# Optimization experiments

Measured on AMD Instinct MI355X. Metric: run time of the kernel, lower is better.

The kernel has to match this reference:

```python
import jax, jax.numpy as jnp
import numpy as np
from jax import lax

# Surrogate spike: forward = Heaviside, backward = g / (1 + 5|x|)^2
@jax.custom_vjp
def spike_fn(x):
    return (x >= 0).astype(x.dtype)

def _spk_fwd(x):
    return spike_fn(x), x

def _spk_bwd(x, g):
    return (g / (1.0 + 5.0 * jnp.abs(x)) ** 2,)

spike_fn.defvjp(_spk_fwd, _spk_bwd)

BN_EPS = 1e-5

def _batchnorm(x, scale, bias, mean, var):
    # x: (B, C, T); eval-mode BN with running stats
    inv = scale / jnp.sqrt(var + BN_EPS)
    return x * inv[None, :, None] + (bias - mean * inv)[None, :, None]

def _conv1d(x, w, b, pad):
    y = lax.conv_general_dilated(x, w, (1,), [(pad, pad)],
                                 dimension_numbers=('NCH', 'OIH', 'NCH'))
    return y + b[None, :, None]

def setup_inputs() -> dict:
    key = jax.random.key(0)
    ks = jax.random.split(key, 12)
    B, T, EEG, GEO, TH, H, OUT = 4096, 320, 64, 18, 32, 16, 4
    inp = {
        'x_eeg': jax.random.normal(ks[0], (B, T, EEG), jnp.float32),
        'x_geo': jax.random.normal(ks[1], (B, T, GEO), jnp.float32),
        'conv1_w': jax.random.normal(ks[2], (TH, EEG, 5), jnp.float32) * 0.05,
        'conv1_b': jnp.zeros((TH,), jnp.float32),
        'bn1_s': jnp.ones((TH,), jnp.float32),
        'bn1_b': jnp.zeros((TH,), jnp.float32),
        'bn1_m': jnp.zeros((TH,), jnp.float32),
        'bn1_v': jnp.ones((TH,), jnp.float32),
        'conv2_w': jax.random.normal(ks[3], (H, TH, 3), jnp.float32) * 0.1,
        'conv2_b': jnp.zeros((H,), jnp.float32),
        'bn2_s': jnp.ones((H,), jnp.float32),
        'bn2_b': jnp.zeros((H,), jnp.float32),
        'bn2_m': jnp.zeros((H,), jnp.float32),
        'bn2_v': jnp.ones((H,), jnp.float32),
        'geo_w': jax.random.normal(ks[4], (H, GEO), jnp.float32) * 0.2,
        'geo_b': jnp.zeros((H,), jnp.float32),
        'gamma': jnp.full((H,), 0.5, jnp.float32),
        'fc1_w': jax.random.normal(ks[5], (64, 160), jnp.float32) * 0.08,
        'fc1_b': jnp.zeros((64,), jnp.float32),
        'fc2_w': jax.random.normal(ks[6], (OUT, 64), jnp.float32) * 0.12,
        'fc2_b': jnp.zeros((OUT,), jnp.float32),
    }
    return inp

def reference(x_eeg, x_geo, conv1_w, conv1_b, bn1_s, bn1_b, bn1_m, bn1_v,
              conv2_w, conv2_b, bn2_s, bn2_b, bn2_m, bn2_v,
              geo_w, geo_b, gamma, fc1_w, fc1_b, fc2_w, fc2_b):
    B, T, _ = x_eeg.shape
    theta_0, beta, tau_a, tau_m = 0.5, 1.8, 0.36, 0.8

    # EEG temporal encoder (eval mode: dropout = identity)
    h = x_eeg.transpose(0, 2, 1)  # (B, 64, T)
    h = jax.nn.relu(_batchnorm(_conv1d(h, conv1_w, conv1_b, 2), bn1_s, bn1_b, bn1_m, bn1_v))
    h = jax.nn.relu(_batchnorm(_conv1d(h, conv2_w, conv2_b, 1), bn2_s, bn2_b, bn2_m, bn2_v))
    eeg_encoded = h.transpose(0, 2, 1)  # (B, T, 16)

    geo_mod = jax.nn.sigmoid(jnp.einsum('bti,hi->bth', x_geo, geo_w) + geo_b)  # (B, T, 16)

    H = eeg_encoded.shape[-1]
    zeros = jnp.zeros((B, H), x_eeg.dtype)
    init = (zeros, zeros, zeros, zeros)  # mem_alif, eta, mem_li, prev_spk

    def step(carry, xs):
        mem_alif, eta, mem_li, prev_spk = carry
        cur_eeg, cur_geo = xs
        eta = tau_a * eta + (1.0 - tau_a) * prev_spk
        theta_t = theta_0 + beta * eta - gamma * cur_geo
        mem_alif = tau_m * mem_alif + cur_eeg
        spk = spike_fn(mem_alif - theta_t)
        mem_alif = mem_alif * (1.0 - spk)
        mem_li = 0.9 * mem_li + spk
        return (mem_alif, eta, mem_li, spk), mem_li

    xs = (eeg_encoded.transpose(1, 0, 2), geo_mod.transpose(1, 0, 2))  # (T, B, 16)
    _, pot = lax.scan(step, init, xs)  # (T, B, 16)

    pot = pot.transpose(1, 2, 0)                 # (B, 16, T)
    windows = pot.reshape(B, H, 10, 32)          # T = 320 = 10*32
    dp_feat = (windows[..., 16:].mean(-1) - windows[..., :16].mean(-1)).reshape(B, -1)  # (B, 160)

    out = jax.nn.relu(dp_feat @ fc1_w.T + fc1_b) @ fc2_w.T + fc2_b  # (B, 4)
    return out
```

## Files before the change

### kernel.cpp

```cpp
#include <hip/hip_runtime.h>
#include <math.h>

#define TB    4096
#define TSEQ  320
#define NEEG  64
#define NTH   32
#define NH    16
#define NGEO  18
#define TILE_T 48
#define NTILES 7
#define XROWS2 54
#define H1ROWS 50

typedef _Float16 f16x8 __attribute__((ext_vector_type(8)));
typedef _Float16 f16x2 __attribute__((ext_vector_type(2)));
typedef float f32x4 __attribute__((ext_vector_type(4)));
#define INV2048 4.8828125e-4f

#define OFF_W1F  0
#define OFF_W2F  10240
#define OFF_B1   11776
#define OFF_B2   11808
#define OFF_GWT  11824
#define OFF_FC1T 12112
#define OFF_FC2T 22352
#define OFF_ZP   22656
#define OFF_E    32768
#define SZ_EC    (TB*TSEQ*NH)
#define OFF_C    (OFF_E + SZ_EC)
#define OFF_DP   (OFF_C + SZ_EC)
#define SZ_DP    (TB*160)
#define REQ_FLOATS ((size_t)OFF_DP + SZ_DP)
#define REQ_BYTES  (REQ_FLOATS * 4)

__global__ void __launch_bounds__(256)
prep_kernel(const float* __restrict__ c1w, const float* __restrict__ c1b,
            const float* __restrict__ s1,  const float* __restrict__ bb1,
            const float* __restrict__ mm1, const float* __restrict__ vv1,
            const float* __restrict__ c2w, const float* __restrict__ c2b,
            const float* __restrict__ s2,  const float* __restrict__ bb2,
            const float* __restrict__ mm2, const float* __restrict__ vv2,
            const float* __restrict__ gw,  const float* __restrict__ fc1w,
            const float* __restrict__ fc2w, float* __restrict__ ws)
{
    const int tid = threadIdx.x;
    _Float16* w1fp = reinterpret_cast<_Float16*>(ws + OFF_W1F);
    _Float16* w2fp = reinterpret_cast<_Float16*>(ws + OFF_W2F);

    for (int d = tid; d < 10240; d += 256) {
        int j = d & 7, l = (d >> 3) & 63, nbk = d >> 9;
        int kk = nbk >> 1, nb = nbk & 1;
        int k = kk >> 1, i = (kk & 1) * 32 + ((l >> 4) * 8) + j;
        int c = nb * 16 + (l & 15);
        float inv = s1[c] / sqrtf(vv1[c] + 1e-5f);
        float wv = c1w[c * 320 + i * 5 + k] * inv;
        _Float16 hi = (_Float16)wv;
        _Float16 lo = (_Float16)((wv - (float)hi) * 2048.f);
        w1fp[((nbk * 2 + 0) * 64 + l) * 8 + j] = hi;
        w1fp[((nbk * 2 + 1) * 64 + l) * 8 + j] = lo;
    }
    for (int d = tid; d < 1536; d += 256) {
        int j = d & 7, l = (d >> 3) & 63, kk2 = d >> 9;
        int c = (l >> 4) * 8 + j;
        int o = l & 15;
        float inv = s2[o] / sqrtf(vv2[o] + 1e-5f);
        float wv = c2w[o * 96 + c * 3 + kk2] * inv;
        _Float16 hi = (_Float16)wv;
        _Float16 lo = (_Float16)((wv - (float)hi) * 2048.f);
        w2fp[((kk2 * 2 + 0) * 64 + l) * 8 + j] = hi;
        w2fp[((kk2 * 2 + 1) * 64 + l) * 8 + j] = lo;
    }
    if (tid < NTH) {
        float inv = s1[tid] / sqrtf(vv1[tid] + 1e-5f);
        ws[OFF_B1 + tid] = c1b[tid] * inv + bb1[tid] - mm1[tid] * inv;
    }
    if (tid < NH) {
        float inv = s2[tid] / sqrtf(vv2[tid] + 1e-5f);
        ws[OFF_B2 + tid] = c2b[tid] * inv + bb2[tid] - mm2[tid] * inv;
    }
    for (int d = tid; d < NGEO * NH; d += 256) {
        int i = d / NH, h = d - i * NH;
        ws[OFF_GWT + d] = gw[h * NGEO + i];
    }
    for (int d = tid; d < 160 * 64; d += 256) {
        int f = d / 64, o = d - f * 64;
        ws[OFF_FC1T + d] = fc1w[o * 160 + f];
    }
    if (tid < 256) {
        int j = tid / 4, o = tid - j * 4;
        ws[OFF_FC2T + tid] = fc2w[o * 64 + j];
    }
    if (tid < 64) ws[OFF_ZP + tid] = 0.f;
}

__global__ void __launch_bounds__(256, 2)
convm_kernel(const float* __restrict__ xeeg, const float* __restrict__ xgeo,
             const float* __restrict__ ws,   const float* __restrict__ geo_b,
             const float* __restrict__ gamma,
             float* __restrict__ E, float* __restrict__ C)
{
    __shared__ __align__(16) float xbuf[2][XROWS2 * 64];
    __shared__ __align__(16) float xg32[14 * 64];
    __shared__ __align__(16) _Float16 w2f[3][2][64][8];
    __shared__ __align__(16) _Float16 h1h[H1ROWS * 32];
    __shared__ __align__(16) _Float16 h1l[H1ROWS * 32];
    __shared__ __align__(16) float gws[NGEO * NH];
    __shared__ float b1s[32], b2s[16], gbs[16], gams[16];

    const int b = blockIdx.x, tid = threadIdx.x;
    const int l = tid & 63, w = tid >> 6;
    const int lrow = l & 15, lkg = l >> 4;
    const int nb = w >> 1, wsub = w & 1;
    const int ug = tid >> 2, hq = tid & 3;

    const float* xb  = xeeg + (size_t)b * TSEQ * NEEG;
    const float* xgb = xgeo + (size_t)b * TSEQ * NGEO;
    const float* zp  = ws + OFF_ZP;

#define STAGE_DMA(buf, t0n) do {                                                     \
        for (int c_ = w; c_ < XROWS2; c_ += 4) {                                     \
            int tg_ = (t0n) - 3 + c_;                                                \
            const float* s_ = (tg_ >= 0 && tg_ < TSEQ)                               \
                              ? (xb + (size_t)tg_ * 64 + l) : zp;                    \
            __builtin_amdgcn_global_load_lds(                                        \
                (const __attribute__((address_space(1))) void*)s_,                   \
                (__attribute__((address_space(3))) void*)&xbuf[(buf)][c_ * 64],      \
                4, 0, 0);                                                            \
        }                                                                            \
        for (int c_ = w; c_ < 14; c_ += 4) {                                         \
            int fo_ = (t0n) * NGEO + c_ * 64;                                        \
            const float* s_ = (fo_ < TSEQ * NGEO) ? (xgb + fo_ + l) : zp;            \
            __builtin_amdgcn_global_load_lds(                                        \
                (const __attribute__((address_space(1))) void*)s_,                   \
                (__attribute__((address_space(3))) void*)&xg32[c_ * 64],             \
                4, 0, 0);                                                            \
        }                                                                            \
    } while (0)

    f16x8 B1h[10], B1l[10];
    {
        const f16x8* wsrc = reinterpret_cast<const f16x8*>(ws + OFF_W1F);
        #pragma unroll
        for (int kk = 0; kk < 10; ++kk) {
            B1h[kk] = wsrc[((kk * 2 + nb) * 2 + 0) * 64 + l];
            B1l[kk] = wsrc[((kk * 2 + nb) * 2 + 1) * 64 + l];
        }
    }
    {
        const float4* s2 = reinterpret_cast<const float4*>(ws + OFF_W2F);
        float4* d2 = reinterpret_cast<float4*>(&w2f[0][0][0][0]);
        for (int p = tid; p < 384; p += 256) d2[p] = s2[p];
        if (tid < 32) b1s[tid] = ws[OFF_B1 + tid];
        if (tid < 16) {
            b2s[tid] = ws[OFF_B2 + tid];
            gbs[tid] = geo_b[tid];
            gams[tid] = gamma[tid];
        }
        for (int p = tid; p < NGEO * NH; p += 256) gws[p] = ws[OFF_GWT + p];
    }
    STAGE_DMA(0, 0);
    __syncthreads();

    for (int jt = 0; jt < NTILES; ++jt) {
        const int t0 = jt * TILE_T;
        const int cur = jt & 1;
        _Float16* xh = reinterpret_cast<_Float16*>(&xbuf[cur][0]);
        _Float16* xl = xh + XROWS2 * 64;

        float2 xr2[7];
        #pragma unroll
        for (int q = 0; q < 7; ++q) {
            int p = tid + q * 256;
            if (p < XROWS2 * 32) {
                int xr = p >> 5, ip = (p & 31) * 2;
                xr2[q] = *reinterpret_cast<const float2*>(&xbuf[cur][xr * 64 + ip]);
            }
        }
        if (ug < TILE_T && t0 + ug < TSEQ) {
            float z0 = gbs[hq * 4 + 0], z1 = gbs[hq * 4 + 1];
            float z2 = gbs[hq * 4 + 2], z3 = gbs[hq * 4 + 3];
            const float* xgr = &xg32[ug * NGEO];
            #pragma unroll
            for (int ii = 0; ii < NGEO; ++ii) {
                float xv = xgr[ii];
                float4 wv = *reinterpret_cast<const float4*>(&gws[ii * 16 + hq * 4]);
                z0 = fmaf(xv, wv.x, z0);
                z1 = fmaf(xv, wv.y, z1);
                z2 = fmaf(xv, wv.z, z2);
                z3 = fmaf(xv, wv.w, z3);
            }
            const int t4o = (t0 + ug) >> 2, tt = ug & 3;
            float* cp = C + (((size_t)t4o * TB + b) * 16 + hq * 4) * 4 + tt;
            cp[0]  = gams[hq * 4 + 0] * (1.f / (1.f + expf(-z0)));
            cp[4]  = gams[hq * 4 + 1] * (1.f / (1.f + expf(-z1)));
            cp[8]  = gams[hq * 4 + 2] * (1.f / (1.f + expf(-z2)));
            cp[12] = gams[hq * 4 + 3] * (1.f / (1.f + expf(-z3)));
        }
        __syncthreads();

        #pragma unroll
        for (int q = 0; q < 7; ++q) {
            int p = tid + q * 256;
            if (p < XROWS2 * 32) {
                int xr = p >> 5, ip = (p & 31) * 2;
                float f0 = xr2[q].x, f1 = xr2[q].y;
                _Float16 h0 = (_Float16)f0, h1v = (_Float16)f1;
                f16x2 vh = {h0, h1v};
                f16x2 vl = {(_Float16)((f0 - (float)h0) * 2048.f),
                            (_Float16)((f1 - (float)h1v) * 2048.f)};
                int idx = xr * 64 + (((ip >> 3) ^ (xr & 7)) << 3) + (ip & 7);
                *reinterpret_cast<f16x2*>(&xh[idx]) = vh;
                *reinterpret_cast<f16x2*>(&xl[idx]) = vl;
            }
        }
        __syncthreads();

        if (jt + 1 < NTILES) STAGE_DMA(cur ^ 1, (jt + 1) * TILE_T);
        __builtin_amdgcn_s_setprio(1);
        {
            const float bia = b1s[nb * 16 + lrow];
            #pragma unroll
            for (int pi = 0; pi < 2; ++pi) {
                const int mb = wsub + pi * 2;
                const int mbase = mb * 16;
                int s = mbase + lrow; if (s > H1ROWS - 1) s = H1ROWS - 1;
                f32x4 aH = {0.f, 0.f, 0.f, 0.f};
                f32x4 aM = aH, aL = aH;
                #pragma unroll
                for (int kk = 0; kk < 10; ++kk) {
                    const int xr = s + (kk >> 1);
                    const int gx = (kk & 1) * 4 + lkg;
                    const int off = xr * 64 + ((gx ^ (xr & 7)) << 3);
                    f16x8 Ah = *reinterpret_cast<const f16x8*>(&xh[off]);
                    f16x8 Al = *reinterpret_cast<const f16x8*>(&xl[off]);
                    aH = __builtin_amdgcn_mfma_f32_16x16x32_f16(Ah, B1h[kk], aH, 0, 0, 0);
                    aM = __builtin_amdgcn_mfma_f32_16x16x32_f16(Ah, B1l[kk], aM, 0, 0, 0);
                    aL = __builtin_amdgcn_mfma_f32_16x16x32_f16(Al, B1h[kk], aL, 0, 0, 0);
                }
                #pragma unroll
                for (int r = 0; r < 4; ++r) {
                    int so = mbase + lkg * 4 + r;
                    if (so < H1ROWS) {
                        int tg = t0 - 1 + so;
                        bool v = (tg >= 0 && tg < TSEQ);
                        float val = v ? fmaxf(fmaf(aM[r] + aL[r], INV2048, aH[r]) + bia, 0.f) : 0.f;
                        int key = (so >> 1) & 3;
                        int g = (nb * 2 + (lrow >> 3)) ^ key;
                        int idx = so * 32 + (g << 3) + (lrow & 7);
                        _Float16 hh = (_Float16)val;
                        h1h[idx] = hh;
                        h1l[idx] = (_Float16)((val - (float)hh) * 2048.f);
                    }
                }
            }
        }
        __builtin_amdgcn_s_setprio(0);
        __syncthreads();

        if (w < 3 && t0 + w * 16 < TSEQ) {
            const int ub = w * 16;
            f32x4 aH = {0.f, 0.f, 0.f, 0.f};
            f32x4 aM = aH, aL = aH;
            __builtin_amdgcn_s_setprio(1);
            #pragma unroll
            for (int kk = 0; kk < 3; ++kk) {
                int srow = ub + lrow + kk;
                int off = srow * 32 + ((lkg ^ ((srow >> 1) & 3)) << 3);
                f16x8 Ah = *reinterpret_cast<const f16x8*>(&h1h[off]);
                f16x8 Al = *reinterpret_cast<const f16x8*>(&h1l[off]);
                f16x8 Bh = *reinterpret_cast<const f16x8*>(&w2f[kk][0][l][0]);
                f16x8 Bl = *reinterpret_cast<const f16x8*>(&w2f[kk][1][l][0]);
                aH = __builtin_amdgcn_mfma_f32_16x16x32_f16(Ah, Bh, aH, 0, 0, 0);
                aM = __builtin_amdgcn_mfma_f32_16x16x32_f16(Ah, Bl, aM, 0, 0, 0);
                aL = __builtin_amdgcn_mfma_f32_16x16x32_f16(Al, Bh, aL, 0, 0, 0);
            }
            __builtin_amdgcn_s_setprio(0);
            const float bia = b2s[lrow];
            float4 ev;
            float* evp = reinterpret_cast<float*>(&ev);
            #pragma unroll
            for (int r = 0; r < 4; ++r)
                evp[r] = fmaxf(fmaf(aM[r] + aL[r], INV2048, aH[r]) + bia, 0.f);
            const int t4o = ((t0 + ub) >> 2) + lkg;
            float* ep = E + (((size_t)t4o * TB + b) * 16 + lrow) * 4;
            *reinterpret_cast<float4*>(ep) = ev;
        }
    }
#undef STAGE_DMA
}

__global__ void __launch_bounds__(256)
scan_kernel(const float* __restrict__ E, const float* __restrict__ C,
            float* __restrict__ DP)
{
    const int tid = threadIdx.x;
    const int h = tid & 15;
    const int b = blockIdx.x * 16 + (tid >> 4);
    const float4* e4 = reinterpret_cast<const float4*>(E);
    const float4* c4 = reinterpret_cast<const float4*>(C);
    const size_t idx = (size_t)b * 16 + h;
    const size_t slab = (size_t)TB * 16;

    float eta = 0.f, memv = 0.f, li = 0.f, ps = 0.f, accF = 0.f, accS = 0.f;
    float4 ev = e4[idx], cv = c4[idx];
    for (int t4 = 0; t4 < 80; ++t4) {
        float4 en, cn;
        if (t4 < 79) { en = e4[(size_t)(t4 + 1) * slab + idx]; cn = c4[(size_t)(t4 + 1) * slab + idx]; }
        const float* evp = reinterpret_cast<const float*>(&ev);
        const float* cvp = reinterpret_cast<const float*>(&cv);
        #pragma unroll
        for (int tt = 0; tt < 4; ++tt) {
            float e = evp[tt], c = cvp[tt];
            eta = 0.36f * eta + 0.64f * ps;
            float theta = 0.5f + 1.8f * eta - c;
            memv = 0.8f * memv + e;
            float spk = (memv - theta >= 0.f) ? 1.f : 0.f;
            memv *= (1.f - spk);
            li = 0.9f * li + spk;
            ps = spk;
            int t = t4 * 4 + tt;
            if (((t >> 4) & 1) == 0) accF += li; else accS += li;
        }
        if ((t4 & 7) == 7) {
            DP[(size_t)b * 160 + h * 10 + (t4 >> 3)] = (accS - accF) * 0.0625f;
            accF = 0.f; accS = 0.f;
        }
        ev = en; cv = cn;
    }
}

__global__ void __launch_bounds__(256)
fc_kernel(const float* __restrict__ DP, const float* __restrict__ ws,
          const float* __restrict__ fc1_b, const float* __restrict__ fc2_b,
          float* __restrict__ out)
{
    __shared__ float sh_dp[4][160];
    __shared__ float mid[4][64];
    const int tid = threadIdx.x;
    const int b0 = blockIdx.x * 4;
    for (int p = tid; p < 640; p += 256)
        sh_dp[p / 160][p - (p / 160) * 160] = DP[(size_t)b0 * 160 + p];
    __syncthreads();
    {
        const int bl = tid >> 6, o = tid & 63;
        const float* __restrict__ fc1t = ws + OFF_FC1T;
        float z = fc1_b[o];
        for (int f = 0; f < 160; ++f) z = fmaf(sh_dp[bl][f], fc1t[f * 64 + o], z);
        mid[bl][o] = fmaxf(z, 0.f);
    }
    __syncthreads();
    if (tid < 16) {
        const int bl = tid >> 2, oo = tid & 3;
        const float* __restrict__ fc2t = ws + OFF_FC2T;
        float z = fc2_b[oo];
        #pragma unroll
        for (int jj = 0; jj < 64; ++jj) z = fmaf(mid[bl][jj], fc2t[jj * 4 + oo], z);
        out[(size_t)(b0 + bl) * 4 + oo] = z;
    }
}

extern "C" void kernel_launch(void* const* d_in, const int* in_sizes, int n_in,
                              void* d_out, int out_size, void* d_ws, size_t ws_size,
                              hipStream_t stream)
{
    const float* xeeg = (const float*)d_in[0];
    const float* xgeo = (const float*)d_in[1];
    const float* c1w  = (const float*)d_in[2];
    const float* c1b  = (const float*)d_in[3];
    const float* s1   = (const float*)d_in[4];
    const float* bb1  = (const float*)d_in[5];
    const float* mm1  = (const float*)d_in[6];
    const float* vv1  = (const float*)d_in[7];
    const float* c2w  = (const float*)d_in[8];
    const float* c2b  = (const float*)d_in[9];
    const float* s2   = (const float*)d_in[10];
    const float* bb2  = (const float*)d_in[11];
    const float* mm2  = (const float*)d_in[12];
    const float* vv2  = (const float*)d_in[13];
    const float* gw   = (const float*)d_in[14];
    const float* gb   = (const float*)d_in[15];
    const float* gam  = (const float*)d_in[16];
    const float* fc1w = (const float*)d_in[17];
    const float* fc1b = (const float*)d_in[18];
    const float* fc2w = (const float*)d_in[19];
    const float* fc2b = (const float*)d_in[20];
    float* ws   = (float*)d_ws;
    float* outp = (float*)d_out;

    hipLaunchKernelGGL(prep_kernel, dim3(1), dim3(256), 0, stream,
                       c1w, c1b, s1, bb1, mm1, vv1, c2w, c2b, s2, bb2, mm2, vv2,
                       gw, fc1w, fc2w, ws);

    float* E  = ws + OFF_E;
    float* C  = ws + OFF_C;
    float* DP = ws + OFF_DP;
    hipLaunchKernelGGL(convm_kernel, dim3(TB), dim3(256), 0, stream,
                       xeeg, xgeo, ws, gb, gam, E, C);
    hipLaunchKernelGGL(scan_kernel, dim3(TB / 16), dim3(256), 0, stream,
                       E, C, DP);
    hipLaunchKernelGGL(fc_kernel, dim3(TB / 4), dim3(256), 0, stream,
                       DP, ws, fc1b, fc2b, outp);
}
```

Measured before the change: 337.0 us.

## Fuse spiking scan into conv kernel via LDS and enlarge time tile

Removes the separate scan kernel and the E/C intermediate global buffers. The conv kernel now writes the encoded EEG and geo modulation per tile into LDS, and 16 threads run the recurrent ALIF scan in-block, writing DP directly. The time tile grows from 48 to 64 so five tiles cover the sequence exactly, with an extra conv1 M-block alternated between warps. This saves global write/read traffic of two large tensors, but serializes the scan on 16 lanes inside each block, which may stall the conv pipeline and raise LDS use that could hurt occupancy.

```diff
diff --git a/kernel.cpp b/kernel.cpp
--- a/kernel.cpp
+++ b/kernel.cpp
@@ -7,10 +7,10 @@
 #define NTH   32
 #define NH    16
 #define NGEO  18
-#define TILE_T 48
-#define NTILES 7
-#define XROWS2 54
-#define H1ROWS 50
+#define TILE_T 64
+#define NTILES 5
+#define XROWS2 70
+#define H1ROWS 66
 
 typedef _Float16 f16x8 __attribute__((ext_vector_type(8)));
 typedef _Float16 f16x2 __attribute__((ext_vector_type(2)));
@@ -25,13 +25,7 @@
 #define OFF_FC1T 12112
 #define OFF_FC2T 22352
 #define OFF_ZP   22656
-#define OFF_E    32768
-#define SZ_EC    (TB*TSEQ*NH)
-#define OFF_C    (OFF_E + SZ_EC)
-#define OFF_DP   (OFF_C + SZ_EC)
-#define SZ_DP    (TB*160)
-#define REQ_FLOATS ((size_t)OFF_DP + SZ_DP)
-#define REQ_BYTES  (REQ_FLOATS * 4)
+#define OFF_DPF  32768
 
 __global__ void __launch_bounds__(256)
 prep_kernel(const float* __restrict__ c1w, const float* __restrict__ c1b,
@@ -96,14 +90,15 @@
 __global__ void __launch_bounds__(256, 2)
 convm_kernel(const float* __restrict__ xeeg, const float* __restrict__ xgeo,
              const float* __restrict__ ws,   const float* __restrict__ geo_b,
-             const float* __restrict__ gamma,
-             float* __restrict__ E, float* __restrict__ C)
+             const float* __restrict__ gamma, float* __restrict__ DP)
 {
     __shared__ __align__(16) float xbuf[2][XROWS2 * 64];
-    __shared__ __align__(16) float xg32[14 * 64];
+    __shared__ __align__(16) float xg32[18 * 64];
     __shared__ __align__(16) _Float16 w2f[3][2][64][8];
     __shared__ __align__(16) _Float16 h1h[H1ROWS * 32];
     __shared__ __align__(16) _Float16 h1l[H1ROWS * 32];
+    __shared__ __align__(16) float E_lds[TILE_T][20];
+    __shared__ __align__(16) float C_lds[2][TILE_T][20];
     __shared__ __align__(16) float gws[NGEO * NH];
     __shared__ float b1s[32], b2s[16], gbs[16], gams[16];
 
@@ -127,9 +122,8 @@
                 (__attribute__((address_space(3))) void*)&xbuf[(buf)][c_ * 64],      \
                 4, 0, 0);                                                            \
         }                                                                            \
-        for (int c_ = w; c_ < 14; c_ += 4) {                                         \
-            int fo_ = (t0n) * NGEO + c_ * 64;                                        \
-            const float* s_ = (fo_ < TSEQ * NGEO) ? (xgb + fo_ + l) : zp;            \
+        for (int c_ = w; c_ < 18; c_ += 4) {                                         \
+            const float* s_ = xgb + (size_t)(t0n) * NGEO + c_ * 64 + l;              \
             __builtin_amdgcn_global_load_lds(                                        \
                 (const __attribute__((address_space(1))) void*)s_,                   \
                 (__attribute__((address_space(3))) void*)&xg32[c_ * 64],             \
@@ -158,6 +152,8 @@
         }
         for (int p = tid; p < NGEO * NH; p += 256) gws[p] = ws[OFF_GWT + p];
     }
+    float eta = 0.f, memv = 0.f, li = 0.f, ps = 0.f, accF = 0.f, accS = 0.f;
+
     STAGE_DMA(0, 0);
     __syncthreads();
 
@@ -167,16 +163,16 @@
         _Float16* xh = reinterpret_cast<_Float16*>(&xbuf[cur][0]);
         _Float16* xl = xh + XROWS2 * 64;
 
-        float2 xr2[7];
+        float2 xr2[9];
         #pragma unroll
-        for (int q = 0; q < 7; ++q) {
+        for (int q = 0; q < 9; ++q) {
             int p = tid + q * 256;
             if (p < XROWS2 * 32) {
                 int xr = p >> 5, ip = (p & 31) * 2;
                 xr2[q] = *reinterpret_cast<const float2*>(&xbuf[cur][xr * 64 + ip]);
             }
         }
-        if (ug < TILE_T && t0 + ug < TSEQ) {
+        {
             float z0 = gbs[hq * 4 + 0], z1 = gbs[hq * 4 + 1];
             float z2 = gbs[hq * 4 + 2], z3 = gbs[hq * 4 + 3];
             const float* xgr = &xg32[ug * NGEO];
@@ -189,17 +185,17 @@
                 z2 = fmaf(xv, wv.z, z2);
                 z3 = fmaf(xv, wv.w, z3);
             }
-            const int t4o = (t0 + ug) >> 2, tt = ug & 3;
-            float* cp = C + (((size_t)t4o * TB + b) * 16 + hq * 4) * 4 + tt;
-            cp[0]  = gams[hq * 4 + 0] * (1.f / (1.f + expf(-z0)));
-            cp[4]  = gams[hq * 4 + 1] * (1.f / (1.f + expf(-z1)));
-            cp[8]  = gams[hq * 4 + 2] * (1.f / (1.f + expf(-z2)));
-            cp[12] = gams[hq * 4 + 3] * (1.f / (1.f + expf(-z3)));
+            float4 cv;
+            cv.x = gams[hq * 4 + 0] * (1.f / (1.f + expf(-z0)));
+            cv.y = gams[hq * 4 + 1] * (1.f / (1.f + expf(-z1)));
+            cv.z = gams[hq * 4 + 2] * (1.f / (1.f + expf(-z2)));
+            cv.w = gams[hq * 4 + 3] * (1.f / (1.f + expf(-z3)));
+            *reinterpret_cast<float4*>(&C_lds[cur][ug][hq * 4]) = cv;
         }
         __syncthreads();
 
         #pragma unroll
-        for (int q = 0; q < 7; ++q) {
+        for (int q = 0; q < 9; ++q) {
             int p = tid + q * 256;
             if (p < XROWS2 * 32) {
                 int xr = p >> 5, ip = (p & 31) * 2;
@@ -220,8 +216,9 @@
         {
             const float bia = b1s[nb * 16 + lrow];
             #pragma unroll
-            for (int pi = 0; pi < 2; ++pi) {
-                const int mb = wsub + pi * 2;
+            for (int pi = 0; pi < 3; ++pi) {
+                if (pi == 2 && ((jt & 1) != wsub)) break;
+                const int mb = (pi < 2) ? (wsub + pi * 2) : 4;
                 const int mbase = mb * 16;
                 int s = mbase + lrow; if (s > H1ROWS - 1) s = H1ROWS - 1;
                 f32x4 aH = {0.f, 0.f, 0.f, 0.f};
@@ -257,7 +254,7 @@
         __builtin_amdgcn_s_setprio(0);
         __syncthreads();
 
-        if (w < 3 && t0 + w * 16 < TSEQ) {
+        {
             const int ub = w * 16;
             f32x4 aH = {0.f, 0.f, 0.f, 0.f};
             f32x4 aM = aH, aL = aH;
@@ -276,57 +273,35 @@
             }
             __builtin_amdgcn_s_setprio(0);
             const float bia = b2s[lrow];
-            float4 ev;
-            float* evp = reinterpret_cast<float*>(&ev);
             #pragma unroll
             for (int r = 0; r < 4; ++r)
-                evp[r] = fmaxf(fmaf(aM[r] + aL[r], INV2048, aH[r]) + bia, 0.f);
-            const int t4o = ((t0 + ub) >> 2) + lkg;
-            float* ep = E + (((size_t)t4o * TB + b) * 16 + lrow) * 4;
-            *reinterpret_cast<float4*>(ep) = ev;
+                E_lds[ub + lkg * 4 + r][lrow] =
+                    fmaxf(fmaf(aM[r] + aL[r], INV2048, aH[r]) + bia, 0.f);
+        }
+        __syncthreads();
+
+        if (tid < 16) {
+            const int h = tid;
+            for (int tt = 0; tt < TILE_T; ++tt) {
+                float e = E_lds[tt][h];
+                float c = C_lds[cur][tt][h];
+                eta = 0.36f * eta + 0.64f * ps;
+                float theta = 0.5f + 1.8f * eta - c;
+                memv = 0.8f * memv + e;
+                float spk = (memv - theta >= 0.f) ? 1.f : 0.f;
+                memv *= (1.f - spk);
+                li = 0.9f * li + spk;
+                ps = spk;
+                int t = t0 + tt;
+                if (((t >> 4) & 1) == 0) accF += li; else accS += li;
+                if ((t & 31) == 31) {
+                    DP[(size_t)b * 160 + h * 10 + (t >> 5)] = (accS - accF) * 0.0625f;
+                    accF = 0.f; accS = 0.f;
+                }
+            }
         }
     }
 #undef STAGE_DMA
-}
-
-__global__ void __launch_bounds__(256)
-scan_kernel(const float* __restrict__ E, const float* __restrict__ C,
-            float* __restrict__ DP)
-{
-    const int tid = threadIdx.x;
-    const int h = tid & 15;
-    const int b = blockIdx.x * 16 + (tid >> 4);
-    const float4* e4 = reinterpret_cast<const float4*>(E);
-    const float4* c4 = reinterpret_cast<const float4*>(C);
-    const size_t idx = (size_t)b * 16 + h;
-    const size_t slab = (size_t)TB * 16;
-
-    float eta = 0.f, memv = 0.f, li = 0.f, ps = 0.f, accF = 0.f, accS = 0.f;
-    float4 ev = e4[idx], cv = c4[idx];
-    for (int t4 = 0; t4 < 80; ++t4) {
-        float4 en, cn;
-        if (t4 < 79) { en = e4[(size_t)(t4 + 1) * slab + idx]; cn = c4[(size_t)(t4 + 1) * slab + idx]; }
-        const float* evp = reinterpret_cast<const float*>(&ev);
-        const float* cvp = reinterpret_cast<const float*>(&cv);
-        #pragma unroll
-        for (int tt = 0; tt < 4; ++tt) {
-            float e = evp[tt], c = cvp[tt];
-            eta = 0.36f * eta + 0.64f * ps;
-            float theta = 0.5f + 1.8f * eta - c;
-            memv = 0.8f * memv + e;
-            float spk = (memv - theta >= 0.f) ? 1.f : 0.f;
-            memv *= (1.f - spk);
-            li = 0.9f * li + spk;
-            ps = spk;
-            int t = t4 * 4 + tt;
-            if (((t >> 4) & 1) == 0) accF += li; else accS += li;
-        }
-        if ((t4 & 7) == 7) {
-            DP[(size_t)b * 160 + h * 10 + (t4 >> 3)] = (accS - accF) * 0.0625f;
-            accF = 0.f; accS = 0.f;
-        }
-        ev = en; cv = cn;
-    }
 }
 
 __global__ void __launch_bounds__(256)
@@ -391,13 +366,9 @@
                        c1w, c1b, s1, bb1, mm1, vv1, c2w, c2b, s2, bb2, mm2, vv2,
                        gw, fc1w, fc2w, ws);
 
-    float* E  = ws + OFF_E;
-    float* C  = ws + OFF_C;
-    float* DP = ws + OFF_DP;
+    float* DP = ws + OFF_DPF;
     hipLaunchKernelGGL(convm_kernel, dim3(TB), dim3(256), 0, stream,
-                       xeeg, xgeo, ws, gb, gam, E, C);
-    hipLaunchKernelGGL(scan_kernel, dim3(TB / 16), dim3(256), 0, stream,
-                       E, C, DP);
+                       xeeg, xgeo, ws, gb, gam, DP);
     hipLaunchKernelGGL(fc_kernel, dim3(TB / 4), dim3(256), 0, stream,
                        DP, ws, fc1b, fc2b, outp);
 }
```

Result: slower. 397.2 us (+17.9%).
